# Kernel tuning notes

Measured on AMD Instinct MI355X. Metric: run time of the kernel, lower is better.

The kernel has to match this reference:

```python
import jax, jax.numpy as jnp
import numpy as np

N = 50000      # nodes
E = 800000     # edges (avg degree 16)
D_IN, D_H, D_OUT = 128, 128, 64
EPS = 1e-5


def setup_inputs() -> dict:
    key = jax.random.key(0)
    ks = jax.random.split(key, 6)
    feat = jax.random.normal(ks[0], (N, D_IN), dtype=jnp.float32)
    # Consistent CSR adjacency: sorted destination rows -> nodePointer via searchsorted
    rows = np.sort(np.asarray(jax.random.randint(ks[1], (E,), 0, N, dtype=jnp.int32)))
    edge_rows = jnp.asarray(rows, dtype=jnp.int32)              # [E] destination node per edge
    nodePointer = jnp.asarray(np.searchsorted(rows, np.arange(N + 1)), dtype=jnp.int32)  # [N+1]
    edgeList = jax.random.randint(ks[2], (E,), 0, N, dtype=jnp.int32)  # [E] source (column) indices
    def glorot(k, i, o):
        return jax.random.normal(k, (i, o), dtype=jnp.float32) * (1.0 / np.sqrt(i)).astype(np.float32)
    W0 = glorot(ks[3], D_IN, D_H)
    W1 = glorot(ks[4], D_H, D_H)
    W2 = glorot(ks[5], D_H, D_OUT)
    return {"feat": feat, "W0": W0, "W1": W1, "W2": W2,
            "nodePointer": nodePointer, "edgeList": edgeList, "edge_rows": edge_rows}


def _layer_norm(x):
    # Fresh nn.LayerNorm each forward in the original => weight=1, bias=0
    mu = jnp.mean(x, axis=-1, keepdims=True)
    var = jnp.mean(jnp.square(x - mu), axis=-1, keepdims=True)
    return (x - mu) * jax.lax.rsqrt(var + EPS)


def reference(feat, W0, W1, W2, nodePointer, edgeList, edge_rows):
    h = feat
    Ws = [W0, W1, W2]
    n_layers = len(Ws)
    for l, W in enumerate(Ws):
        xw = h @ W                      # [N, d_out] dense GEMM
        msg = xw[edgeList]              # [E, d_out] gather source-node features
        h = jax.ops.segment_sum(msg, edge_rows, num_segments=N)  # SpMM: A @ (h W)
        h = _layer_norm(h)
        if l != n_layers - 1:
            h = jax.nn.relu(h)
    return h
```

## Files before the change

kernel.cpp:

```cpp
#include <hip/hip_runtime.h>
#include <cstddef>


typedef __attribute__((ext_vector_type(8))) short bf16x8;
typedef __attribute__((ext_vector_type(4))) float floatx4;
typedef __attribute__((ext_vector_type(4))) unsigned int uintx4;
typedef __attribute__((ext_vector_type(2))) unsigned int uintx2;

static __device__ __forceinline__ unsigned int f2bf(float f) {
    union { float f; unsigned int u; } v; v.f = f;
    unsigned int u = v.u;
    u += 0x7fffu + ((u >> 16) & 1u);
    return u >> 16;
}
static __device__ __forceinline__ float bf_lo(unsigned int p) {
    union { unsigned int u; float f; } v; v.u = p << 16; return v.f;
}
static __device__ __forceinline__ float bf_hi(unsigned int p) {
    union { unsigned int u; float f; } v; v.u = p & 0xffff0000u; return v.f;
}
static __device__ __forceinline__ void acc8(float* a, uintx4 v) {
    a[0] += bf_lo(v.x); a[1] += bf_hi(v.x);
    a[2] += bf_lo(v.y); a[3] += bf_hi(v.y);
    a[4] += bf_lo(v.z); a[5] += bf_hi(v.z);
    a[6] += bf_lo(v.w); a[7] += bf_hi(v.w);
}
static __device__ __forceinline__ void acc4(float* a, uintx2 v) {
    a[0] += bf_lo(v.x); a[1] += bf_hi(v.x);
    a[2] += bf_lo(v.y); a[3] += bf_hi(v.y);
}

__global__ __launch_bounds__(256) void cvt_w(const float* __restrict__ W0,
                                             const float* __restrict__ W1,
                                             const float* __restrict__ W2,
                                             unsigned int* __restrict__ WtF) {
    const int m = blockIdx.x >> 4;
    const int slice = blockIdx.x & 15;
    const float* W = (m == 0) ? W0 : (m == 1) ? W1 : W2;
    const int ncols = (m == 2) ? 64 : 128;
    unsigned int* dst = WtF + m * 128 * 64;
    const int total = ncols * 64;
    for (int idx = slice * 256 + threadIdx.x; idx < total; idx += 16 * 256) {
        const int j    = idx & 3;
        const int lane = (idx >> 2) & 63;
        const int s    = (idx >> 8) & 3;
        const int t    = idx >> 10;
        const int mcol = lane & 15;
        const int quad = lane >> 4;
        const int n = t * 16 + mcol;
        const int k = s * 32 + quad * 8 + 2 * j;
        unsigned int lo = f2bf(W[(size_t)k * ncols + n]);
        unsigned int hi = f2bf(W[(size_t)(k + 1) * ncols + n]);
        dst[idx] = (hi << 16) | lo;
    }
}

template <int NCOLS, bool A_FP32>
__global__ __launch_bounds__(64) void gemm_mfma(const void* __restrict__ Av,
                                                const unsigned int* __restrict__ Wt,
                                                unsigned int* __restrict__ C,
                                                int M) {
    const int lane = threadIdx.x;
    const int row0 = blockIdx.x * 16;
    const int quad = lane >> 4;
    const int mcol = lane & 15;

    constexpr int NT = NCOLS / 16;
    floatx4 acc[NT];
    #pragma unroll
    for (int t = 0; t < NT; ++t) acc[t] = (floatx4){0.f, 0.f, 0.f, 0.f};

    int aidx = row0 + mcol; if (aidx >= M) aidx = M - 1;
    const float*        arowF = (const float*)Av + (size_t)aidx * 128 + quad * 8;
    const unsigned int* afrag = (const unsigned int*)Av + (size_t)blockIdx.x * 1024 + lane * 4;
    const unsigned int* bbase = Wt + lane * 4;

    #pragma unroll
    for (int s = 0; s < 4; ++s) {
        bf16x8 a;
        if constexpr (A_FP32) {
            float4 fa = *(const float4*)(arowF + s * 32);
            float4 fb = *(const float4*)(arowF + s * 32 + 4);
            uintx4 ap;
            ap.x = (f2bf(fa.y) << 16) | f2bf(fa.x);
            ap.y = (f2bf(fa.w) << 16) | f2bf(fa.z);
            ap.z = (f2bf(fb.y) << 16) | f2bf(fb.x);
            ap.w = (f2bf(fb.w) << 16) | f2bf(fb.z);
            a = __builtin_bit_cast(bf16x8, ap);
        } else {
            uintx4 ap = *(const uintx4*)(afrag + s * 256);
            a = __builtin_bit_cast(bf16x8, ap);
        }
        #pragma unroll
        for (int t = 0; t < NT; ++t) {
            uintx4 bp = *(const uintx4*)(bbase + t * 1024 + s * 256);
            bf16x8 b = __builtin_bit_cast(bf16x8, bp);
            acc[t] = __builtin_amdgcn_mfma_f32_16x16x32_bf16(a, b, acc[t], 0, 0, 0);
        }
    }

    const int rowStride = NCOLS >> 1;
    #pragma unroll
    for (int t = 0; t < NT; ++t) {
        #pragma unroll
        for (int r = 0; r < 4; ++r) {
            unsigned int mybf = f2bf(acc[t][r]);
            unsigned int pair = __shfl_xor(mybf, 1, 64);
            int orow = row0 + quad * 4 + r;
            if (orow < M && (mcol & 1) == 0) {
                unsigned int packed = (pair << 16) | mybf;
                C[(size_t)orow * rowStride + t * 8 + (mcol >> 1)] = packed;
            }
        }
    }
}

template <int NCOLS_OUT>
__global__ __launch_bounds__(256) void agg_gemm(const unsigned int* __restrict__ xw,
                                                const int* __restrict__ ptr,
                                                const int* __restrict__ col,
                                                const unsigned int* __restrict__ Wt,
                                                unsigned int* __restrict__ C,
                                                int N, int Emax ) {
    __shared__ unsigned int lds[1024];
    const int tile = blockIdx.x;
    const int wave = threadIdx.x >> 6;
    const int lane = threadIdx.x & 63;
    const int g  = lane >> 4;
    const int sl = lane & 15;

    int s0[4], len[4];
    int maxlen = 0;
    #pragma unroll
    for (int n = 0; n < 4; ++n) {
        const int node = tile * 16 + wave * 4 + n;
        const int nc = node < N ? node : N - 1;
        const int a = ptr[nc];
        const int b = node < N ? ptr[nc + 1] : a;
        s0[n] = a; len[n] = b - a;
        maxlen = max(maxlen, len[n]);
    }

    float acc[4][8] = {};
    const unsigned int* base = xw + sl * 4;

    if (maxlen > 0) {
        #define LOADCOL(dst, OFF)                                            \
            _Pragma("unroll")                                                \
            for (int n = 0; n < 4; ++n) {                                    \
                int idx = (OFF) + g;                                         \
                idx = idx < len[n] ? idx : 0;                                \
                int ei = s0[n] + idx;                                        \
                ei = ei < Emax ? ei : Emax;                                  \
                dst[n] = col[ei];                                            \
            }
        #define GATHER4(dst, c)                                              \
            _Pragma("unroll")                                                \
            for (int n = 0; n < 4; ++n)                                      \
                dst[n] = *(const uintx4*)(base + (size_t)c[n] * 64);
        #define ACCUM4(v, OFF)                                               \
            _Pragma("unroll")                                                \
            for (int n = 0; n < 4; ++n)                                      \
                if ((OFF) + g < len[n]) acc8(acc[n], v[n]);

        int cA[4], cB[4], cC[4], cD[4];
        uintx4 vA[4], vB[4];
        LOADCOL(cA, 0)
        LOADCOL(cB, 4)
        GATHER4(vA, cA)
        LOADCOL(cC, 8)
        GATHER4(vB, cB)
        LOADCOL(cD, 12)

        const int rounds = (maxlen + 7) & ~7;
        for (int off = 0; off < rounds; off += 8) {
            ACCUM4(vA, off)
            GATHER4(vA, cC)
            LOADCOL(cC, off + 16)
            ACCUM4(vB, off + 4)
            GATHER4(vB, cD)
            LOADCOL(cD, off + 20)
        }
        #undef LOADCOL
        #undef GATHER4
        #undef ACCUM4
    }

    #pragma unroll
    for (int n = 0; n < 4; ++n) {
        const int m = wave * 4 + n;
        float a8[8];
        #pragma unroll
        for (int j = 0; j < 8; ++j) {
            float t = acc[n][j];
            t += __shfl_xor(t, 16, 64);
            t += __shfl_xor(t, 32, 64);
            a8[j] = t;
        }
        float s1 = 0.f, s2 = 0.f;
        #pragma unroll
        for (int j = 0; j < 8; ++j) { s1 += a8[j]; s2 += a8[j] * a8[j]; }
        #pragma unroll
        for (int mm = 8; mm >= 1; mm >>= 1) {
            s1 += __shfl_xor(s1, mm, 64);
            s2 += __shfl_xor(s2, mm, 64);
        }
        const float mean = s1 * (1.0f / 128.0f);
        const float var  = s2 * (1.0f / 128.0f) - mean * mean;
        const float inv  = rsqrtf(var + 1e-5f);

        if (g == 0) {
            float o[8];
            #pragma unroll
            for (int j = 0; j < 8; ++j)
                o[j] = fmaxf((a8[j] - mean) * inv, 0.f);
            uintx4 p;
            p.x = (f2bf(o[1]) << 16) | f2bf(o[0]);
            p.y = (f2bf(o[3]) << 16) | f2bf(o[2]);
            p.z = (f2bf(o[5]) << 16) | f2bf(o[4]);
            p.w = (f2bf(o[7]) << 16) | f2bf(o[6]);
            *(uintx4*)(lds + (sl >> 2) * 256 + (sl & 3) * 64 + m * 4) = p;
        }
    }
    __syncthreads();

    constexpr int WT = NCOLS_OUT / 64;
    const int quad = lane >> 4;
    const int mcol = lane & 15;
    floatx4 macc[WT];
    #pragma unroll
    for (int t = 0; t < WT; ++t) macc[t] = (floatx4){0.f, 0.f, 0.f, 0.f};

    const unsigned int* bbase = Wt + lane * 4;
    #pragma unroll
    for (int s4 = 0; s4 < 4; ++s4) {
        uintx4 ap = *(const uintx4*)(lds + s4 * 256 + lane * 4);
        bf16x8 a = __builtin_bit_cast(bf16x8, ap);
        #pragma unroll
        for (int tt = 0; tt < WT; ++tt) {
            const int t = wave * WT + tt;
            uintx4 bp = *(const uintx4*)(bbase + t * 1024 + s4 * 256);
            bf16x8 b = __builtin_bit_cast(bf16x8, bp);
            macc[tt] = __builtin_amdgcn_mfma_f32_16x16x32_bf16(a, b, macc[tt], 0, 0, 0);
        }
    }

    const int rowStride = NCOLS_OUT >> 1;
    #pragma unroll
    for (int tt = 0; tt < WT; ++tt) {
        const int t = wave * WT + tt;
        #pragma unroll
        for (int r = 0; r < 4; ++r) {
            unsigned int mybf = f2bf(macc[tt][r]);
            unsigned int pair = __shfl_xor(mybf, 1, 64);
            const int orow = tile * 16 + quad * 4 + r;
            if (orow < N && (mcol & 1) == 0) {
                unsigned int packed = (pair << 16) | mybf;
                C[(size_t)orow * rowStride + t * 8 + (mcol >> 1)] = packed;
            }
        }
    }
}

__global__ __launch_bounds__(256) void agg_ln64(const unsigned int* __restrict__ xw,
                                                const int* __restrict__ ptr,
                                                const int* __restrict__ col,
                                                float* __restrict__ out,
                                                int N, int Emax) {
    const int tile = blockIdx.x;
    const int wave = threadIdx.x >> 6;
    const int lane = threadIdx.x & 63;
    const int g  = lane >> 4;
    const int sl = lane & 15;

    int s0[4], len[4];
    int maxlen = 0;
    #pragma unroll
    for (int n = 0; n < 4; ++n) {
        const int node = tile * 16 + wave * 4 + n;
        const int nc = node < N ? node : N - 1;
        const int a = ptr[nc];
        const int b = node < N ? ptr[nc + 1] : a;
        s0[n] = a; len[n] = b - a;
        maxlen = max(maxlen, len[n]);
    }

    float acc[4][4] = {};
    const unsigned int* base = xw + sl * 2;

    if (maxlen > 0) {
        #define LOADCOL(dst, OFF)                                            \
            _Pragma("unroll")                                                \
            for (int n = 0; n < 4; ++n) {                                    \
                int idx = (OFF) + g;                                         \
                idx = idx < len[n] ? idx : 0;                                \
                int ei = s0[n] + idx;                                        \
                ei = ei < Emax ? ei : Emax;                                  \
                dst[n] = col[ei];                                            \
            }
        #define GATHER2(dst, c)                                              \
            _Pragma("unroll")                                                \
            for (int n = 0; n < 4; ++n)                                      \
                dst[n] = *(const uintx2*)(base + (size_t)c[n] * 32);
        #define ACCUM2(v, OFF)                                               \
            _Pragma("unroll")                                                \
            for (int n = 0; n < 4; ++n)                                      \
                if ((OFF) + g < len[n]) acc4(acc[n], v[n]);

        int cA[4], cB[4], cC[4], cD[4];
        uintx2 vA[4], vB[4];
        LOADCOL(cA, 0)
        LOADCOL(cB, 4)
        GATHER2(vA, cA)
        LOADCOL(cC, 8)
        GATHER2(vB, cB)
        LOADCOL(cD, 12)

        const int rounds = (maxlen + 7) & ~7;
        for (int off = 0; off < rounds; off += 8) {
            ACCUM2(vA, off)
            GATHER2(vA, cC)
            LOADCOL(cC, off + 16)
            ACCUM2(vB, off + 4)
            GATHER2(vB, cD)
            LOADCOL(cD, off + 20)
        }
        #undef LOADCOL
        #undef GATHER2
        #undef ACCUM2
    }

    #pragma unroll
    for (int n = 0; n < 4; ++n) {
        const int node = tile * 16 + wave * 4 + n;
        float a4[4];
        #pragma unroll
        for (int j = 0; j < 4; ++j) {
            float t = acc[n][j];
            t += __shfl_xor(t, 16, 64);
            t += __shfl_xor(t, 32, 64);
            a4[j] = t;
        }
        float s1 = 0.f, s2 = 0.f;
        #pragma unroll
        for (int j = 0; j < 4; ++j) { s1 += a4[j]; s2 += a4[j] * a4[j]; }
        #pragma unroll
        for (int mm = 8; mm >= 1; mm >>= 1) {
            s1 += __shfl_xor(s1, mm, 64);
            s2 += __shfl_xor(s2, mm, 64);
        }
        const float mean = s1 * (1.0f / 64.0f);
        const float var  = s2 * (1.0f / 64.0f) - mean * mean;
        const float inv  = rsqrtf(var + 1e-5f);

        if (g == 0 && node < N) {
            float4 o;
            o.x = (a4[0] - mean) * inv;
            o.y = (a4[1] - mean) * inv;
            o.z = (a4[2] - mean) * inv;
            o.w = (a4[3] - mean) * inv;
            *(float4*)(out + (size_t)node * 64 + sl * 4) = o;
        }
    }
}

extern "C" void kernel_launch(void* const* d_in, const int* in_sizes, int n_in,
                              void* d_out, int out_size, void* d_ws, size_t ws_size,
                              hipStream_t stream) {
    const float* feat = (const float*)d_in[0];
    const float* W0   = (const float*)d_in[1];
    const float* W1   = (const float*)d_in[2];
    const float* W2   = (const float*)d_in[3];
    const int*   ptr  = (const int*)d_in[4];
    const int*   col  = (const int*)d_in[5];

    const int N = in_sizes[4] - 1;
    const int E = in_sizes[5];
    const int Emax = E - 1;

    unsigned int* buf0 = (unsigned int*)d_ws;
    unsigned int* buf1 = buf0 + (size_t)N * 64;
    unsigned int* WtP  = buf1 + (size_t)N * 64;
    float*        out  = (float*)d_out;

    const int tileBlocks = (N + 15) / 16;

    cvt_w<<<48, 256, 0, stream>>>(W0, W1, W2, WtP);

    gemm_mfma<128, true><<<tileBlocks, 64, 0, stream>>>(feat, WtP, buf0, N);
    agg_gemm<128><<<tileBlocks, 256, 0, stream>>>(buf0, ptr, col, WtP + 128 * 64, buf1, N, Emax);
    agg_gemm<64><<<tileBlocks, 256, 0, stream>>>(buf1, ptr, col, WtP + 2 * 128 * 64, buf0, N, Emax);
    agg_ln64<<<tileBlocks, 256, 0, stream>>>(buf0, ptr, col, out, N, Emax);
}
```

Measured before the change: 189.0 us.

## Gather neighbor rows via async global-to-LDS ring buffer with bpermute column indices

Replaces the register-pipelined neighbor gathers in the aggregation kernels with a 9-slot per-wave LDS ring filled by global_load_lds, keeping up to 8 loads in flight under explicit vmcnt waits. Column indices for each group of 4 nodes are loaded once per wave and distributed with ds_bpermute. A zero row in workspace replaces per-edge masking for out-of-range slots. The final 64-wide layer is also re-laid out to 8 lanes per row with 16-byte loads. This adds LDS use (36KB per block) that may lower occupancy, and falls back to a simple loop when the 4 nodes have more than 128 edges in total.

```diff
diff --git a/kernel.cpp b/kernel.cpp
--- a/kernel.cpp
+++ b/kernel.cpp
@@ -5,7 +5,6 @@
 typedef __attribute__((ext_vector_type(8))) short bf16x8;
 typedef __attribute__((ext_vector_type(4))) float floatx4;
 typedef __attribute__((ext_vector_type(4))) unsigned int uintx4;
-typedef __attribute__((ext_vector_type(2))) unsigned int uintx2;
 
 static __device__ __forceinline__ unsigned int f2bf(float f) {
     union { float f; unsigned int u; } v; v.f = f;
@@ -25,15 +24,19 @@
     a[4] += bf_lo(v.z); a[5] += bf_hi(v.z);
     a[6] += bf_lo(v.w); a[7] += bf_hi(v.w);
 }
-static __device__ __forceinline__ void acc4(float* a, uintx2 v) {
-    a[0] += bf_lo(v.x); a[1] += bf_hi(v.x);
-    a[2] += bf_lo(v.y); a[3] += bf_hi(v.y);
+
+static __device__ __forceinline__ void gload16(const void* g, void* l) {
+    __builtin_amdgcn_global_load_lds(
+        (const __attribute__((address_space(1))) void*)g,
+        (__attribute__((address_space(3))) void*)l, 16, 0, 0);
 }
 
 __global__ __launch_bounds__(256) void cvt_w(const float* __restrict__ W0,
                                              const float* __restrict__ W1,
                                              const float* __restrict__ W2,
-                                             unsigned int* __restrict__ WtF) {
+                                             unsigned int* __restrict__ WtF,
+                                             unsigned int* __restrict__ zrow) {
+    if (blockIdx.x == 0 && threadIdx.x < 64) zrow[threadIdx.x] = 0u;
     const int m = blockIdx.x >> 4;
     const int slice = blockIdx.x & 15;
     const float* W = (m == 0) ? W0 : (m == 1) ? W1 : W2;
@@ -115,77 +118,99 @@
     }
 }
 
+template <int ROWB>
+static __device__ __forceinline__ void gather_ring(
+        const unsigned int* __restrict__ xw,
+        const int* __restrict__ ptr,
+        const int* __restrict__ col,
+        const unsigned int* __restrict__ zrow,
+        unsigned int* ringw, int lane, int first, int N, int Emax,
+        float acc[4][8]) {
+    constexpr int SLANES = ROWB / 16;
+    constexpr int OSTEP  = 64 / SLANES;
+    const int g  = lane / SLANES;
+    const int sl = lane % SLANES;
+
+    int s0[4], len[4];
+    int maxlen = 0;
+    #pragma unroll
+    for (int n = 0; n < 4; ++n) {
+        const int nn = first + n;
+        const int nc = nn < N ? nn : N - 1;
+        const int a = ptr[nc];
+        const int b = nn < N ? ptr[nc + 1] : a;
+        s0[n] = a; len[n] = b - a;
+        maxlen = max(maxlen, len[n]);
+    }
+    const int base = s0[0];
+    const int Ltot = s0[3] + len[3] - base;
+
+    if (Ltot <= 128) {
+        const int colv0 = col[min(base + lane, Emax)];
+        const int colv1 = col[min(base + 64 + lane, Emax)];
+        const int rounds = (maxlen + OSTEP - 1) / OSTEP;
+
+        auto issue = [&](int s0n, int lenn, int s_, int slot_) {
+            const int idx = (s_ >> 2) * OSTEP + g;
+            const int p = (s0n - base) + idx;
+            const int cc0 = __builtin_amdgcn_ds_bpermute(p << 2, colv0);
+            const int cc1 = __builtin_amdgcn_ds_bpermute((p - 64) << 2, colv1);
+            const unsigned int cc = (p < 64) ? (unsigned int)cc0 : (unsigned int)cc1;
+            const char* ga = (idx < lenn)
+                ? ((const char*)xw + (size_t)cc * ROWB + sl * 16)
+                : ((const char*)zrow + sl * 16);
+            gload16(ga, (void*)(ringw + slot_ * 256));
+        };
+
+        #pragma unroll
+        for (int i = 0; i < 8; ++i) issue(s0[i & 3], len[i & 3], i, i);
+
+        int si = 8, sc = 0;
+        for (int r = 0; r < rounds; ++r) {
+            #pragma unroll
+            for (int n = 0; n < 4; ++n) {
+                asm volatile("s_waitcnt vmcnt(7)" ::: "memory");
+                uintx4 v = *(const uintx4*)(ringw + sc * 256 + lane * 4);
+                acc8(acc[n], v);
+                __builtin_amdgcn_sched_barrier(0);
+                issue(s0[n], len[n], r * 4 + n + 8, si);
+                si = (si == 8) ? 0 : si + 1;
+                sc = (sc == 8) ? 0 : sc + 1;
+            }
+        }
+        asm volatile("s_waitcnt vmcnt(0)" ::: "memory");
+    } else {
+        #pragma unroll
+        for (int n = 0; n < 4; ++n) {
+            for (int i = s0[n] + g; i < s0[n] + len[n]; i += OSTEP) {
+                const unsigned int c = (unsigned int)col[i];
+                uintx4 v = *(const uintx4*)((const char*)xw + (size_t)c * ROWB + sl * 16);
+                acc8(acc[n], v);
+            }
+        }
+    }
+}
+
 template <int NCOLS_OUT>
 __global__ __launch_bounds__(256) void agg_gemm(const unsigned int* __restrict__ xw,
                                                 const int* __restrict__ ptr,
                                                 const int* __restrict__ col,
                                                 const unsigned int* __restrict__ Wt,
                                                 unsigned int* __restrict__ C,
-                                                int N, int Emax ) {
-    __shared__ unsigned int lds[1024];
+                                                const unsigned int* __restrict__ zrow,
+                                                int N, int Emax) {
+    __shared__ unsigned int ring[4][9][256];
+    __shared__ unsigned int atile[1024];
     const int tile = blockIdx.x;
     const int wave = threadIdx.x >> 6;
     const int lane = threadIdx.x & 63;
+
+    float acc[4][8] = {};
+    gather_ring<256>(xw, ptr, col, zrow, &ring[wave][0][0], lane,
+                     tile * 16 + wave * 4, N, Emax, acc);
+
     const int g  = lane >> 4;
     const int sl = lane & 15;
-
-    int s0[4], len[4];
-    int maxlen = 0;
-    #pragma unroll
-    for (int n = 0; n < 4; ++n) {
-        const int node = tile * 16 + wave * 4 + n;
-        const int nc = node < N ? node : N - 1;
-        const int a = ptr[nc];
-        const int b = node < N ? ptr[nc + 1] : a;
-        s0[n] = a; len[n] = b - a;
-        maxlen = max(maxlen, len[n]);
-    }
-
-    float acc[4][8] = {};
-    const unsigned int* base = xw + sl * 4;
-
-    if (maxlen > 0) {
-        #define LOADCOL(dst, OFF)                                            \
-            _Pragma("unroll")                                                \
-            for (int n = 0; n < 4; ++n) {                                    \
-                int idx = (OFF) + g;                                         \
-                idx = idx < len[n] ? idx : 0;                                \
-                int ei = s0[n] + idx;                                        \
-                ei = ei < Emax ? ei : Emax;                                  \
-                dst[n] = col[ei];                                            \
-            }
-        #define GATHER4(dst, c)                                              \
-            _Pragma("unroll")                                                \
-            for (int n = 0; n < 4; ++n)                                      \
-                dst[n] = *(const uintx4*)(base + (size_t)c[n] * 64);
-        #define ACCUM4(v, OFF)                                               \
-            _Pragma("unroll")                                                \
-            for (int n = 0; n < 4; ++n)                                      \
-                if ((OFF) + g < len[n]) acc8(acc[n], v[n]);
-
-        int cA[4], cB[4], cC[4], cD[4];
-        uintx4 vA[4], vB[4];
-        LOADCOL(cA, 0)
-        LOADCOL(cB, 4)
-        GATHER4(vA, cA)
-        LOADCOL(cC, 8)
-        GATHER4(vB, cB)
-        LOADCOL(cD, 12)
-
-        const int rounds = (maxlen + 7) & ~7;
-        for (int off = 0; off < rounds; off += 8) {
-            ACCUM4(vA, off)
-            GATHER4(vA, cC)
-            LOADCOL(cC, off + 16)
-            ACCUM4(vB, off + 4)
-            GATHER4(vB, cD)
-            LOADCOL(cD, off + 20)
-        }
-        #undef LOADCOL
-        #undef GATHER4
-        #undef ACCUM4
-    }
-
     #pragma unroll
     for (int n = 0; n < 4; ++n) {
         const int m = wave * 4 + n;
@@ -219,7 +244,7 @@
             p.y = (f2bf(o[3]) << 16) | f2bf(o[2]);
             p.z = (f2bf(o[5]) << 16) | f2bf(o[4]);
             p.w = (f2bf(o[7]) << 16) | f2bf(o[6]);
-            *(uintx4*)(lds + (sl >> 2) * 256 + (sl & 3) * 64 + m * 4) = p;
+            *(uintx4*)(atile + (sl >> 2) * 256 + (sl & 3) * 64 + m * 4) = p;
         }
     }
     __syncthreads();
@@ -234,7 +259,7 @@
     const unsigned int* bbase = Wt + lane * 4;
     #pragma unroll
     for (int s4 = 0; s4 < 4; ++s4) {
-        uintx4 ap = *(const uintx4*)(lds + s4 * 256 + lane * 4);
+        uintx4 ap = *(const uintx4*)(atile + s4 * 256 + lane * 4);
         bf16x8 a = __builtin_bit_cast(bf16x8, ap);
         #pragma unroll
         for (int tt = 0; tt < WT; ++tt) {
@@ -266,86 +291,35 @@
                                                 const int* __restrict__ ptr,
                                                 const int* __restrict__ col,
                                                 float* __restrict__ out,
+                                                const unsigned int* __restrict__ zrow,
                                                 int N, int Emax) {
-    const int tile = blockIdx.x;
+    __shared__ unsigned int ring[4][9][256];
     const int wave = threadIdx.x >> 6;
     const int lane = threadIdx.x & 63;
-    const int g  = lane >> 4;
-    const int sl = lane & 15;
-
-    int s0[4], len[4];
-    int maxlen = 0;
+
+    float acc[4][8] = {};
+    gather_ring<128>(xw, ptr, col, zrow, &ring[wave][0][0], lane,
+                     blockIdx.x * 16 + wave * 4, N, Emax, acc);
+
+    const int g  = lane >> 3;
+    const int sl = lane & 7;
     #pragma unroll
     for (int n = 0; n < 4; ++n) {
-        const int node = tile * 16 + wave * 4 + n;
-        const int nc = node < N ? node : N - 1;
-        const int a = ptr[nc];
-        const int b = node < N ? ptr[nc + 1] : a;
-        s0[n] = a; len[n] = b - a;
-        maxlen = max(maxlen, len[n]);
-    }
-
-    float acc[4][4] = {};
-    const unsigned int* base = xw + sl * 2;
-
-    if (maxlen > 0) {
-        #define LOADCOL(dst, OFF)                                            \
-            _Pragma("unroll")                                                \
-            for (int n = 0; n < 4; ++n) {                                    \
-                int idx = (OFF) + g;                                         \
-                idx = idx < len[n] ? idx : 0;                                \
-                int ei = s0[n] + idx;                                        \
-                ei = ei < Emax ? ei : Emax;                                  \
-                dst[n] = col[ei];                                            \
-            }
-        #define GATHER2(dst, c)                                              \
-            _Pragma("unroll")                                                \
-            for (int n = 0; n < 4; ++n)                                      \
-                dst[n] = *(const uintx2*)(base + (size_t)c[n] * 32);
-        #define ACCUM2(v, OFF)                                               \
-            _Pragma("unroll")                                                \
-            for (int n = 0; n < 4; ++n)                                      \
-                if ((OFF) + g < len[n]) acc4(acc[n], v[n]);
-
-        int cA[4], cB[4], cC[4], cD[4];
-        uintx2 vA[4], vB[4];
-        LOADCOL(cA, 0)
-        LOADCOL(cB, 4)
-        GATHER2(vA, cA)
-        LOADCOL(cC, 8)
-        GATHER2(vB, cB)
-        LOADCOL(cD, 12)
-
-        const int rounds = (maxlen + 7) & ~7;
-        for (int off = 0; off < rounds; off += 8) {
-            ACCUM2(vA, off)
-            GATHER2(vA, cC)
-            LOADCOL(cC, off + 16)
-            ACCUM2(vB, off + 4)
-            GATHER2(vB, cD)
-            LOADCOL(cD, off + 20)
-        }
-        #undef LOADCOL
-        #undef GATHER2
-        #undef ACCUM2
-    }
-
-    #pragma unroll
-    for (int n = 0; n < 4; ++n) {
-        const int node = tile * 16 + wave * 4 + n;
-        float a4[4];
-        #pragma unroll
-        for (int j = 0; j < 4; ++j) {
+        const int node = blockIdx.x * 16 + wave * 4 + n;
+        float a8[8];
+        #pragma unroll
+        for (int j = 0; j < 8; ++j) {
             float t = acc[n][j];
+            t += __shfl_xor(t, 8, 64);
             t += __shfl_xor(t, 16, 64);
             t += __shfl_xor(t, 32, 64);
-            a4[j] = t;
+            a8[j] = t;
         }
         float s1 = 0.f, s2 = 0.f;
         #pragma unroll
-        for (int j = 0; j < 4; ++j) { s1 += a4[j]; s2 += a4[j] * a4[j]; }
-        #pragma unroll
-        for (int mm = 8; mm >= 1; mm >>= 1) {
+        for (int j = 0; j < 8; ++j) { s1 += a8[j]; s2 += a8[j] * a8[j]; }
+        #pragma unroll
+        for (int mm = 4; mm >= 1; mm >>= 1) {
             s1 += __shfl_xor(s1, mm, 64);
             s2 += __shfl_xor(s2, mm, 64);
         }
@@ -354,12 +328,17 @@
         const float inv  = rsqrtf(var + 1e-5f);
 
         if (g == 0 && node < N) {
-            float4 o;
-            o.x = (a4[0] - mean) * inv;
-            o.y = (a4[1] - mean) * inv;
-            o.z = (a4[2] - mean) * inv;
-            o.w = (a4[3] - mean) * inv;
-            *(float4*)(out + (size_t)node * 64 + sl * 4) = o;
+            float4 o0, o1;
+            o0.x = (a8[0] - mean) * inv;
+            o0.y = (a8[1] - mean) * inv;
+            o0.z = (a8[2] - mean) * inv;
+            o0.w = (a8[3] - mean) * inv;
+            o1.x = (a8[4] - mean) * inv;
+            o1.y = (a8[5] - mean) * inv;
+            o1.z = (a8[6] - mean) * inv;
+            o1.w = (a8[7] - mean) * inv;
+            *(float4*)(out + (size_t)node * 64 + sl * 8)     = o0;
+            *(float4*)(out + (size_t)node * 64 + sl * 8 + 4) = o1;
         }
     }
 }
@@ -381,14 +360,15 @@
     unsigned int* buf0 = (unsigned int*)d_ws;
     unsigned int* buf1 = buf0 + (size_t)N * 64;
     unsigned int* WtP  = buf1 + (size_t)N * 64;
+    unsigned int* zrow = WtP + 3 * 128 * 64;
     float*        out  = (float*)d_out;
 
     const int tileBlocks = (N + 15) / 16;
 
-    cvt_w<<<48, 256, 0, stream>>>(W0, W1, W2, WtP);
+    cvt_w<<<48, 256, 0, stream>>>(W0, W1, W2, WtP, zrow);
 
     gemm_mfma<128, true><<<tileBlocks, 64, 0, stream>>>(feat, WtP, buf0, N);
-    agg_gemm<128><<<tileBlocks, 256, 0, stream>>>(buf0, ptr, col, WtP + 128 * 64, buf1, N, Emax);
-    agg_gemm<64><<<tileBlocks, 256, 0, stream>>>(buf1, ptr, col, WtP + 2 * 128 * 64, buf0, N, Emax);
-    agg_ln64<<<tileBlocks, 256, 0, stream>>>(buf0, ptr, col, out, N, Emax);
-}
+    agg_gemm<128><<<tileBlocks, 256, 0, stream>>>(buf0, ptr, col, WtP + 128 * 64, buf1, zrow, N, Emax);
+    agg_gemm<64><<<tileBlocks, 256, 0, stream>>>(buf1, ptr, col, WtP + 2 * 128 * 64, buf0, zrow, N, Emax);
+    agg_ln64<<<tileBlocks, 256, 0, stream>>>(buf0, ptr, col, out, zrow, N, Emax);
+}
```

After: 250.4 us. 1.33x slower.

## Bucket-sort each node's neighbor list by source index block for gather locality

Applied to the files above, without the earlier changes.

Adds a per-node pass, fused into the weight-conversion kernel, that reorders each row's column indices into 25 buckets by source index (c>>11). All three aggregation kernels then use the reordered list. Because the aggregation is a sum, the result is unchanged, and gathers from nearby source rows should get better cache locality. The sort costs 25 passes over each row's edges, run serially by one thread per node, on every call. The unused bf16 A-fragment path in gemm_mfma is also removed.

```diff
diff --git a/kernel.cpp b/kernel.cpp
--- a/kernel.cpp
+++ b/kernel.cpp
@@ -30,28 +30,47 @@
     a[2] += bf_lo(v.y); a[3] += bf_hi(v.y);
 }
 
-__global__ __launch_bounds__(256) void cvt_w(const float* __restrict__ W0,
-                                             const float* __restrict__ W1,
-                                             const float* __restrict__ W2,
-                                             unsigned int* __restrict__ WtF) {
-    const int m = blockIdx.x >> 4;
-    const int slice = blockIdx.x & 15;
-    const float* W = (m == 0) ? W0 : (m == 1) ? W1 : W2;
-    const int ncols = (m == 2) ? 64 : 128;
-    unsigned int* dst = WtF + m * 128 * 64;
-    const int total = ncols * 64;
-    for (int idx = slice * 256 + threadIdx.x; idx < total; idx += 16 * 256) {
-        const int j    = idx & 3;
-        const int lane = (idx >> 2) & 63;
-        const int s    = (idx >> 8) & 3;
-        const int t    = idx >> 10;
-        const int mcol = lane & 15;
-        const int quad = lane >> 4;
-        const int n = t * 16 + mcol;
-        const int k = s * 32 + quad * 8 + 2 * j;
-        unsigned int lo = f2bf(W[(size_t)k * ncols + n]);
-        unsigned int hi = f2bf(W[(size_t)(k + 1) * ncols + n]);
-        dst[idx] = (hi << 16) | lo;
+__global__ __launch_bounds__(256) void cvt_sort(const float* __restrict__ W0,
+                                                const float* __restrict__ W1,
+                                                const float* __restrict__ W2,
+                                                unsigned int* __restrict__ WtF,
+                                                const int* __restrict__ ptr,
+                                                const int* __restrict__ col,
+                                                int* __restrict__ col2,
+                                                int N) {
+    if (blockIdx.x < 48) {
+        const int m = blockIdx.x >> 4;
+        const int slice = blockIdx.x & 15;
+        const float* W = (m == 0) ? W0 : (m == 1) ? W1 : W2;
+        const int ncols = (m == 2) ? 64 : 128;
+        unsigned int* dst = WtF + m * 128 * 64;
+        const int total = ncols * 64;
+        for (int idx = slice * 256 + threadIdx.x; idx < total; idx += 16 * 256) {
+            const int j    = idx & 3;
+            const int lane = (idx >> 2) & 63;
+            const int s    = (idx >> 8) & 3;
+            const int t    = idx >> 10;
+            const int mcol = lane & 15;
+            const int quad = lane >> 4;
+            const int n = t * 16 + mcol;
+            const int k = s * 32 + quad * 8 + 2 * j;
+            unsigned int lo = f2bf(W[(size_t)k * ncols + n]);
+            unsigned int hi = f2bf(W[(size_t)(k + 1) * ncols + n]);
+            dst[idx] = (hi << 16) | lo;
+        }
+    } else {
+        const int node = (blockIdx.x - 48) * 256 + threadIdx.x;
+        if (node < N) {
+            const int s = ptr[node];
+            const int e = ptr[node + 1];
+            int pos = s;
+            for (int b = 0; b < 25; ++b) {
+                for (int i = s; i < e; ++i) {
+                    const int c = col[i];
+                    if ((c >> 11) == b) col2[pos++] = c;
+                }
+            }
+        }
     }
 }
 
@@ -72,25 +91,18 @@
 
     int aidx = row0 + mcol; if (aidx >= M) aidx = M - 1;
     const float*        arowF = (const float*)Av + (size_t)aidx * 128 + quad * 8;
-    const unsigned int* afrag = (const unsigned int*)Av + (size_t)blockIdx.x * 1024 + lane * 4;
     const unsigned int* bbase = Wt + lane * 4;
 
     #pragma unroll
     for (int s = 0; s < 4; ++s) {
-        bf16x8 a;
-        if constexpr (A_FP32) {
-            float4 fa = *(const float4*)(arowF + s * 32);
-            float4 fb = *(const float4*)(arowF + s * 32 + 4);
-            uintx4 ap;
-            ap.x = (f2bf(fa.y) << 16) | f2bf(fa.x);
-            ap.y = (f2bf(fa.w) << 16) | f2bf(fa.z);
-            ap.z = (f2bf(fb.y) << 16) | f2bf(fb.x);
-            ap.w = (f2bf(fb.w) << 16) | f2bf(fb.z);
-            a = __builtin_bit_cast(bf16x8, ap);
-        } else {
-            uintx4 ap = *(const uintx4*)(afrag + s * 256);
-            a = __builtin_bit_cast(bf16x8, ap);
-        }
+        float4 fa = *(const float4*)(arowF + s * 32);
+        float4 fb = *(const float4*)(arowF + s * 32 + 4);
+        uintx4 ap;
+        ap.x = (f2bf(fa.y) << 16) | f2bf(fa.x);
+        ap.y = (f2bf(fa.w) << 16) | f2bf(fa.z);
+        ap.z = (f2bf(fb.y) << 16) | f2bf(fb.x);
+        ap.w = (f2bf(fb.w) << 16) | f2bf(fb.z);
+        bf16x8 a = __builtin_bit_cast(bf16x8, ap);
         #pragma unroll
         for (int t = 0; t < NT; ++t) {
             uintx4 bp = *(const uintx4*)(bbase + t * 1024 + s * 256);
@@ -381,14 +393,15 @@
     unsigned int* buf0 = (unsigned int*)d_ws;
     unsigned int* buf1 = buf0 + (size_t)N * 64;
     unsigned int* WtP  = buf1 + (size_t)N * 64;
+    int*          col2 = (int*)(WtP + 3 * 128 * 64);
     float*        out  = (float*)d_out;
 
-    const int tileBlocks = (N + 15) / 16;
-
-    cvt_w<<<48, 256, 0, stream>>>(W0, W1, W2, WtP);
-
-    gemm_mfma<128, true><<<tileBlocks, 64, 0, stream>>>(feat, WtP, buf0, N);
-    agg_gemm<128><<<tileBlocks, 256, 0, stream>>>(buf0, ptr, col, WtP + 128 * 64, buf1, N, Emax);
-    agg_gemm<64><<<tileBlocks, 256, 0, stream>>>(buf1, ptr, col, WtP + 2 * 128 * 64, buf0, N, Emax);
-    agg_ln64<<<tileBlocks, 256, 0, stream>>>(buf0, ptr, col, out, N, Emax);
-}
+    const int tiles = (N + 15) / 16;
+    const int sortBlocks = (N + 255) / 256;
+
+    cvt_sort<<<48 + sortBlocks, 256, 0, stream>>>(W0, W1, W2, WtP, ptr, col, col2, N);
+    gemm_mfma<128, true><<<tiles, 64, 0, stream>>>(feat, WtP, buf0, N);
+    agg_gemm<128><<<tiles, 256, 0, stream>>>(buf0, ptr, col2, WtP + 128 * 64, buf1, N, Emax);
+    agg_gemm<64><<<tiles, 256, 0, stream>>>(buf1, ptr, col2, WtP + 2 * 128 * 64, buf0, N, Emax);
+    agg_ln64<<<tiles, 256, 0, stream>>>(buf0, ptr, col2, out, N, Emax);
+}
```

New measurement: 317.5 us. 68.0% more time.

## Store intermediate features in column-sliced planes and gather one dword per lane

Applied to the files above, without the earlier changes.

Intermediate bf16 feature buffers move from row-major layout to a column-sliced layout: separate planes of 16 dwords (64 bytes) per node. The aggregation kernels loop over planes, and each lane gathers a single dword per edge instead of a 16- or 8-byte vector. The idea is to shrink the scattered-gather footprint per pass so that each plane fits better in cache. In exchange, the column-index reads and loop overhead are repeated once per plane, and the LDS and output write patterns change to match.

```diff
diff --git a/kernel.cpp b/kernel.cpp
--- a/kernel.cpp
+++ b/kernel.cpp
@@ -5,7 +5,6 @@
 typedef __attribute__((ext_vector_type(8))) short bf16x8;
 typedef __attribute__((ext_vector_type(4))) float floatx4;
 typedef __attribute__((ext_vector_type(4))) unsigned int uintx4;
-typedef __attribute__((ext_vector_type(2))) unsigned int uintx2;
 
 static __device__ __forceinline__ unsigned int f2bf(float f) {
     union { float f; unsigned int u; } v; v.f = f;
@@ -18,16 +17,6 @@
 }
 static __device__ __forceinline__ float bf_hi(unsigned int p) {
     union { unsigned int u; float f; } v; v.u = p & 0xffff0000u; return v.f;
-}
-static __device__ __forceinline__ void acc8(float* a, uintx4 v) {
-    a[0] += bf_lo(v.x); a[1] += bf_hi(v.x);
-    a[2] += bf_lo(v.y); a[3] += bf_hi(v.y);
-    a[4] += bf_lo(v.z); a[5] += bf_hi(v.z);
-    a[6] += bf_lo(v.w); a[7] += bf_hi(v.w);
-}
-static __device__ __forceinline__ void acc4(float* a, uintx2 v) {
-    a[0] += bf_lo(v.x); a[1] += bf_hi(v.x);
-    a[2] += bf_lo(v.y); a[3] += bf_hi(v.y);
 }
 
 __global__ __launch_bounds__(256) void cvt_w(const float* __restrict__ W0,
@@ -55,42 +44,35 @@
     }
 }
 
-template <int NCOLS, bool A_FP32>
-__global__ __launch_bounds__(64) void gemm_mfma(const void* __restrict__ Av,
-                                                const unsigned int* __restrict__ Wt,
-                                                unsigned int* __restrict__ C,
-                                                int M) {
+__global__ __launch_bounds__(64) void gemm0(const float* __restrict__ feat,
+                                            const unsigned int* __restrict__ Wt,
+                                            unsigned int* __restrict__ C,
+                                            int M) {
     const int lane = threadIdx.x;
     const int row0 = blockIdx.x * 16;
     const int quad = lane >> 4;
     const int mcol = lane & 15;
-
-    constexpr int NT = NCOLS / 16;
+    const size_t qN = (size_t)M * 16;
+
+    constexpr int NT = 8;
     floatx4 acc[NT];
     #pragma unroll
     for (int t = 0; t < NT; ++t) acc[t] = (floatx4){0.f, 0.f, 0.f, 0.f};
 
     int aidx = row0 + mcol; if (aidx >= M) aidx = M - 1;
-    const float*        arowF = (const float*)Av + (size_t)aidx * 128 + quad * 8;
-    const unsigned int* afrag = (const unsigned int*)Av + (size_t)blockIdx.x * 1024 + lane * 4;
+    const float*        arowF = feat + (size_t)aidx * 128 + quad * 8;
     const unsigned int* bbase = Wt + lane * 4;
 
     #pragma unroll
     for (int s = 0; s < 4; ++s) {
-        bf16x8 a;
-        if constexpr (A_FP32) {
-            float4 fa = *(const float4*)(arowF + s * 32);
-            float4 fb = *(const float4*)(arowF + s * 32 + 4);
-            uintx4 ap;
-            ap.x = (f2bf(fa.y) << 16) | f2bf(fa.x);
-            ap.y = (f2bf(fa.w) << 16) | f2bf(fa.z);
-            ap.z = (f2bf(fb.y) << 16) | f2bf(fb.x);
-            ap.w = (f2bf(fb.w) << 16) | f2bf(fb.z);
-            a = __builtin_bit_cast(bf16x8, ap);
-        } else {
-            uintx4 ap = *(const uintx4*)(afrag + s * 256);
-            a = __builtin_bit_cast(bf16x8, ap);
-        }
+        float4 fa = *(const float4*)(arowF + s * 32);
+        float4 fb = *(const float4*)(arowF + s * 32 + 4);
+        uintx4 ap;
+        ap.x = (f2bf(fa.y) << 16) | f2bf(fa.x);
+        ap.y = (f2bf(fa.w) << 16) | f2bf(fa.z);
+        ap.z = (f2bf(fb.y) << 16) | f2bf(fb.x);
+        ap.w = (f2bf(fb.w) << 16) | f2bf(fb.z);
+        bf16x8 a = __builtin_bit_cast(bf16x8, ap);
         #pragma unroll
         for (int t = 0; t < NT; ++t) {
             uintx4 bp = *(const uintx4*)(bbase + t * 1024 + s * 256);
@@ -99,7 +81,7 @@
         }
     }
 
-    const int rowStride = NCOLS >> 1;
+    const int mc2 = mcol >> 1;
     #pragma unroll
     for (int t = 0; t < NT; ++t) {
         #pragma unroll
@@ -109,7 +91,8 @@
             int orow = row0 + quad * 4 + r;
             if (orow < M && (mcol & 1) == 0) {
                 unsigned int packed = (pair << 16) | mybf;
-                C[(size_t)orow * rowStride + t * 8 + (mcol >> 1)] = packed;
+                const int idx = t * 8 + mc2;
+                C[(size_t)(idx >> 4) * qN + (size_t)orow * 16 + (idx & 15)] = packed;
             }
         }
     }
@@ -128,6 +111,7 @@
     const int lane = threadIdx.x & 63;
     const int g  = lane >> 4;
     const int sl = lane & 15;
+    const size_t qN = (size_t)N * 16;
 
     int s0[4], len[4];
     int maxlen = 0;
@@ -142,7 +126,6 @@
     }
 
     float acc[4][8] = {};
-    const unsigned int* base = xw + sl * 4;
 
     if (maxlen > 0) {
         #define LOADCOL(dst, OFF)                                            \
@@ -154,36 +137,43 @@
                 ei = ei < Emax ? ei : Emax;                                  \
                 dst[n] = col[ei];                                            \
             }
-        #define GATHER4(dst, c)                                              \
+        #define GATHER1(dst, c)                                              \
             _Pragma("unroll")                                                \
             for (int n = 0; n < 4; ++n)                                      \
-                dst[n] = *(const uintx4*)(base + (size_t)c[n] * 64);
-        #define ACCUM4(v, OFF)                                               \
+                dst[n] = baseq[(size_t)c[n] * 16];
+        #define ACCUM1(v, OFF)                                               \
             _Pragma("unroll")                                                \
             for (int n = 0; n < 4; ++n)                                      \
-                if ((OFF) + g < len[n]) acc8(acc[n], v[n]);
-
-        int cA[4], cB[4], cC[4], cD[4];
-        uintx4 vA[4], vB[4];
-        LOADCOL(cA, 0)
-        LOADCOL(cB, 4)
-        GATHER4(vA, cA)
-        LOADCOL(cC, 8)
-        GATHER4(vB, cB)
-        LOADCOL(cD, 12)
-
-        const int rounds = (maxlen + 7) & ~7;
-        for (int off = 0; off < rounds; off += 8) {
-            ACCUM4(vA, off)
-            GATHER4(vA, cC)
-            LOADCOL(cC, off + 16)
-            ACCUM4(vB, off + 4)
-            GATHER4(vB, cD)
-            LOADCOL(cD, off + 20)
+                if ((OFF) + g < len[n]) {                                    \
+                    acc[n][2 * q]     += bf_lo(v[n]);                        \
+                    acc[n][2 * q + 1] += bf_hi(v[n]);                        \
+                }
+
+        #pragma unroll
+        for (int q = 0; q < 4; ++q) {
+            const unsigned int* baseq = xw + (size_t)q * qN + sl;
+            int cA[4], cB[4], cC[4], cD[4];
+            unsigned int vA[4], vB[4];
+            LOADCOL(cA, 0)
+            LOADCOL(cB, 4)
+            GATHER1(vA, cA)
+            LOADCOL(cC, 8)
+            GATHER1(vB, cB)
+            LOADCOL(cD, 12)
+
+            const int rounds = (maxlen + 7) & ~7;
+            for (int off = 0; off < rounds; off += 8) {
+                ACCUM1(vA, off)
+                GATHER1(vA, cC)
+                LOADCOL(cC, off + 16)
+                ACCUM1(vB, off + 4)
+                GATHER1(vB, cD)
+                LOADCOL(cD, off + 20)
+            }
         }
         #undef LOADCOL
-        #undef GATHER4
-        #undef ACCUM4
+        #undef GATHER1
+        #undef ACCUM1
     }
 
     #pragma unroll
@@ -209,18 +199,11 @@
         const float var  = s2 * (1.0f / 128.0f) - mean * mean;
         const float inv  = rsqrtf(var + 1e-5f);
 
-        if (g == 0) {
-            float o[8];
-            #pragma unroll
-            for (int j = 0; j < 8; ++j)
-                o[j] = fmaxf((a8[j] - mean) * inv, 0.f);
-            uintx4 p;
-            p.x = (f2bf(o[1]) << 16) | f2bf(o[0]);
-            p.y = (f2bf(o[3]) << 16) | f2bf(o[2]);
-            p.z = (f2bf(o[5]) << 16) | f2bf(o[4]);
-            p.w = (f2bf(o[7]) << 16) | f2bf(o[6]);
-            *(uintx4*)(lds + (sl >> 2) * 256 + (sl & 3) * 64 + m * 4) = p;
-        }
+        const float e0 = (g == 0) ? a8[0] : (g == 1) ? a8[2] : (g == 2) ? a8[4] : a8[6];
+        const float e1 = (g == 0) ? a8[1] : (g == 1) ? a8[3] : (g == 2) ? a8[5] : a8[7];
+        const float o0 = fmaxf((e0 - mean) * inv, 0.f);
+        const float o1 = fmaxf((e1 - mean) * inv, 0.f);
+        lds[g * 256 + (sl >> 2) * 64 + m * 4 + (sl & 3)] = (f2bf(o1) << 16) | f2bf(o0);
     }
     __syncthreads();
 
@@ -245,7 +228,7 @@
         }
     }
 
-    const int rowStride = NCOLS_OUT >> 1;
+    const int mc2 = mcol >> 1;
     #pragma unroll
     for (int tt = 0; tt < WT; ++tt) {
         const int t = wave * WT + tt;
@@ -256,7 +239,8 @@
             const int orow = tile * 16 + quad * 4 + r;
             if (orow < N && (mcol & 1) == 0) {
                 unsigned int packed = (pair << 16) | mybf;
-                C[(size_t)orow * rowStride + t * 8 + (mcol >> 1)] = packed;
+                const int idx = t * 8 + mc2;
+                C[(size_t)(idx >> 4) * qN + (size_t)orow * 16 + (idx & 15)] = packed;
             }
         }
     }
@@ -272,6 +256,7 @@
     const int lane = threadIdx.x & 63;
     const int g  = lane >> 4;
     const int sl = lane & 15;
+    const size_t hN = (size_t)N * 16;
 
     int s0[4], len[4];
     int maxlen = 0;
@@ -286,7 +271,6 @@
     }
 
     float acc[4][4] = {};
-    const unsigned int* base = xw + sl * 2;
 
     if (maxlen > 0) {
         #define LOADCOL(dst, OFF)                                            \
@@ -298,36 +282,43 @@
                 ei = ei < Emax ? ei : Emax;                                  \
                 dst[n] = col[ei];                                            \
             }
-        #define GATHER2(dst, c)                                              \
+        #define GATHER1(dst, c)                                              \
             _Pragma("unroll")                                                \
             for (int n = 0; n < 4; ++n)                                      \
-                dst[n] = *(const uintx2*)(base + (size_t)c[n] * 32);
-        #define ACCUM2(v, OFF)                                               \
+                dst[n] = baseh[(size_t)c[n] * 16];
+        #define ACCUM1(v, OFF)                                               \
             _Pragma("unroll")                                                \
             for (int n = 0; n < 4; ++n)                                      \
-                if ((OFF) + g < len[n]) acc4(acc[n], v[n]);
-
-        int cA[4], cB[4], cC[4], cD[4];
-        uintx2 vA[4], vB[4];
-        LOADCOL(cA, 0)
-        LOADCOL(cB, 4)
-        GATHER2(vA, cA)
-        LOADCOL(cC, 8)
-        GATHER2(vB, cB)
-        LOADCOL(cD, 12)
-
-        const int rounds = (maxlen + 7) & ~7;
-        for (int off = 0; off < rounds; off += 8) {
-            ACCUM2(vA, off)
-            GATHER2(vA, cC)
-            LOADCOL(cC, off + 16)
-            ACCUM2(vB, off + 4)
-            GATHER2(vB, cD)
-            LOADCOL(cD, off + 20)
+                if ((OFF) + g < len[n]) {                                    \
+                    acc[n][2 * h]     += bf_lo(v[n]);                        \
+                    acc[n][2 * h + 1] += bf_hi(v[n]);                        \
+                }
+
+        #pragma unroll
+        for (int h = 0; h < 2; ++h) {
+            const unsigned int* baseh = xw + (size_t)h * hN + sl;
+            int cA[4], cB[4], cC[4], cD[4];
+            unsigned int vA[4], vB[4];
+            LOADCOL(cA, 0)
+            LOADCOL(cB, 4)
+            GATHER1(vA, cA)
+            LOADCOL(cC, 8)
+            GATHER1(vB, cB)
+            LOADCOL(cD, 12)
+
+            const int rounds = (maxlen + 7) & ~7;
+            for (int off = 0; off < rounds; off += 8) {
+                ACCUM1(vA, off)
+                GATHER1(vA, cC)
+                LOADCOL(cC, off + 16)
+                ACCUM1(vB, off + 4)
+                GATHER1(vB, cD)
+                LOADCOL(cD, off + 20)
+            }
         }
         #undef LOADCOL
-        #undef GATHER2
-        #undef ACCUM2
+        #undef GATHER1
+        #undef ACCUM1
     }
 
     #pragma unroll
@@ -353,13 +344,13 @@
         const float var  = s2 * (1.0f / 64.0f) - mean * mean;
         const float inv  = rsqrtf(var + 1e-5f);
 
-        if (g == 0 && node < N) {
-            float4 o;
-            o.x = (a4[0] - mean) * inv;
-            o.y = (a4[1] - mean) * inv;
-            o.z = (a4[2] - mean) * inv;
-            o.w = (a4[3] - mean) * inv;
-            *(float4*)(out + (size_t)node * 64 + sl * 4) = o;
+        const float e0 = (g == 0) ? a4[0] : a4[2];
+        const float e1 = (g == 0) ? a4[1] : a4[3];
+        if (g < 2 && node < N) {
+            float2 o;
+            o.x = (e0 - mean) * inv;
+            o.y = (e1 - mean) * inv;
+            *(float2*)(out + (size_t)node * 64 + g * 32 + sl * 2) = o;
         }
     }
 }
@@ -383,12 +374,11 @@
     unsigned int* WtP  = buf1 + (size_t)N * 64;
     float*        out  = (float*)d_out;
 
-    const int tileBlocks = (N + 15) / 16;
+    const int tiles = (N + 15) / 16;
 
     cvt_w<<<48, 256, 0, stream>>>(W0, W1, W2, WtP);
-
-    gemm_mfma<128, true><<<tileBlocks, 64, 0, stream>>>(feat, WtP, buf0, N);
-    agg_gemm<128><<<tileBlocks, 256, 0, stream>>>(buf0, ptr, col, WtP + 128 * 64, buf1, N, Emax);
-    agg_gemm<64><<<tileBlocks, 256, 0, stream>>>(buf1, ptr, col, WtP + 2 * 128 * 64, buf0, N, Emax);
-    agg_ln64<<<tileBlocks, 256, 0, stream>>>(buf0, ptr, col, out, N, Emax);
-}
+    gemm0<<<tiles, 64, 0, stream>>>(feat, WtP, buf0, N);
+    agg_gemm<128><<<tiles, 256, 0, stream>>>(buf0, ptr, col, WtP + 128 * 64, buf1, N, Emax);
+    agg_gemm<64><<<tiles, 256, 0, stream>>>(buf1, ptr, col, WtP + 2 * 128 * 64, buf0, N, Emax);
+    agg_ln64<<<tiles, 256, 0, stream>>>(buf0, ptr, col, out, N, Emax);
+}
```

Measured after the change: 250.0 us. 1.32x slower.
